# Performance work log

Hardware: AMD Instinct MI355X
Metric: run time of the kernel (lower is better)

## Reference

```python
import jax, jax.numpy as jnp
import numpy as np

# dims
B, T, HID = 2, 2048, 2048
HK, HV, DK, DV, KW = 16, 32, 128, 128, 4
KEY_DIM = HK * DK          # 2048
VAL_DIM = HV * DV          # 4096
CONV_DIM = 2 * KEY_DIM + VAL_DIM  # 8192
EPS = 1e-6


def setup_inputs() -> dict:
    key = jax.random.key(0)
    ks = jax.random.split(key, 10)
    s = 0.02
    return {
        "x": jax.random.normal(ks[0], (B, T, HID), jnp.float32),
        "input_pos": jnp.arange(T, dtype=jnp.int64),
        "W_qkv": jax.random.normal(ks[1], (CONV_DIM, HID), jnp.float32) * s,
        "W_z": jax.random.normal(ks[2], (VAL_DIM, HID), jnp.float32) * s,
        "W_b": jax.random.normal(ks[3], (HV, HID), jnp.float32) * s,
        "W_a": jax.random.normal(ks[4], (HV, HID), jnp.float32) * s,
        "conv_w": jax.random.normal(ks[5], (CONV_DIM, 1, KW), jnp.float32) * 0.2,
        "dt_bias": jnp.ones((HV,), jnp.float32),
        "A_log": jnp.log(jax.random.uniform(ks[6], (HV,), jnp.float32, 1e-3, 16.0)),
        "norm_weight": jnp.ones((DV,), jnp.float32),
        "W_out": jax.random.normal(ks[7], (HID, VAL_DIM), jnp.float32) * s,
    }


def _l2norm(t):
    n = jnp.sqrt(jnp.sum(t * t, axis=-1, keepdims=True))
    return t / jnp.maximum(n, 1e-12)


def _gdn_scan(q, k, v, g, beta):
    # per-batch: q,k [T,HV,DK], v [T,HV,DV], g,beta [T,HV]
    scale = DK ** -0.5
    def step(S, inp):  # S: [HV, DK, DV]
        qt, kt, vt, gt, bt = inp
        S = S * jnp.exp(gt)[:, None, None]
        kv = jnp.einsum('hk,hkv->hv', kt, S)
        S = S + jnp.einsum('hk,hv->hkv', kt, bt[:, None] * (vt - kv))
        o = jnp.einsum('hk,hkv->hv', qt * scale, S)
        return S, o
    S0 = jnp.zeros((HV, DK, DV), q.dtype)
    _, o = jax.lax.scan(step, S0, (q, k, v, g, beta))
    return o  # [T, HV, DV]


def reference(x, input_pos, W_qkv, W_z, W_b, W_a, conv_w, dt_bias, A_log, norm_weight, W_out):
    # conv_state / recurrent_state buffers start at zero (and input_pos[0]==0 resets them),
    # so the causal conv reduces to left-padded depthwise conv and the scan starts from S=0.
    mixed_qkv = jnp.einsum('bth,ch->btc', x, W_qkv)                    # [B,T,CONV_DIM]
    z = jnp.einsum('bth,vh->btv', x, W_z).reshape(B, T, HV, DV)
    beta = jax.nn.sigmoid(jnp.einsum('bth,nh->btn', x, W_b))           # [B,T,HV]
    a = jnp.einsum('bth,nh->btn', x, W_a)
    g = -jnp.exp(A_log) * jax.nn.softplus(a + dt_bias)                 # [B,T,HV]

    # causal depthwise conv1d over time
    xc = mixed_qkv.transpose(0, 2, 1)                                  # [B,C,T]
    yc = jax.lax.conv_general_dilated(
        xc, conv_w, window_strides=(1,), padding=[(KW - 1, 0)],
        dimension_numbers=('NCH', 'OIH', 'NCH'), feature_group_count=CONV_DIM)
    qkv = jax.nn.silu(yc).transpose(0, 2, 1)                           # [B,T,C]

    q = qkv[..., :KEY_DIM].reshape(B, T, HK, DK)
    k = qkv[..., KEY_DIM:2 * KEY_DIM].reshape(B, T, HK, DK)
    v = qkv[..., 2 * KEY_DIM:].reshape(B, T, HV, DV)
    q = _l2norm(q)
    k = _l2norm(k)
    rep = HV // HK
    q = jnp.repeat(q, rep, axis=2)                                     # [B,T,HV,DK]
    k = jnp.repeat(k, rep, axis=2)

    o = jax.vmap(_gdn_scan)(q, k, v, g, beta)                          # [B,T,HV,DV]

    # gated RMSNorm: RMSNorm(o) * weight * silu(z)
    of = o.astype(jnp.float32)
    normed = of * jax.lax.rsqrt(jnp.mean(of * of, axis=-1, keepdims=True) + EPS)
    out = (norm_weight * normed) * jax.nn.silu(z.astype(jnp.float32))
    out = out.reshape(B, T, VAL_DIM)
    return jnp.einsum('btv,hv->bth', out, W_out)
```

## Files before the change

### kernel.cpp

```cpp
#include <hip/hip_runtime.h>

#define BB 2
#define TT 2048
#define HID 2048
#define HK 16
#define HV 32
#define DK 128
#define DV 128
#define KW 4
#define KEY_DIM 2048
#define VAL_DIM 4096
#define CONV_DIM 8192
#define N1PAD 12544
#define M_ROWS 4096
#define CC 64

typedef __attribute__((ext_vector_type(8))) short short8;
typedef __attribute__((ext_vector_type(8))) unsigned short ushort8;
typedef __attribute__((ext_vector_type(4))) float f32x4;

__device__ __forceinline__ unsigned short f2bf(float f) {
  union { float f; unsigned int u; } v; v.f = f;
  unsigned int r = v.u + 0x7FFFu + ((v.u >> 16) & 1u);
  return (unsigned short)(r >> 16);
}
__device__ __forceinline__ float bf2f(unsigned short u) {
  union { unsigned int u; float f; } v; v.u = ((unsigned int)u) << 16; return v.f;
}

template <int CTRL>
__device__ __forceinline__ float dpp_add(float v) {
  union { float f; int i; } a, b;
  a.f = v;
  b.i = __builtin_amdgcn_update_dpp(0, a.i, CTRL, 0xf, 0xf, true);
  return a.f + b.f;
}
template <int CTRL>
__device__ __forceinline__ int dpp_mov(int v) {
  return __builtin_amdgcn_update_dpp(0, v, CTRL, 0xf, 0xf, true);
}
__device__ __forceinline__ float row16_sum(float v) {
  v = dpp_add<0xB1>(v); v = dpp_add<0x4E>(v);
  v = dpp_add<0x141>(v); v = dpp_add<0x140>(v);
  return v;
}
__device__ __forceinline__ float row8_sum(float v) {
  v = dpp_add<0xB1>(v); v = dpp_add<0x4E>(v); v = dpp_add<0x141>(v);
  return v;
}

__device__ __forceinline__ void gload_lds16(const unsigned short* g, unsigned short* l) {
  __builtin_amdgcn_global_load_lds((const __attribute__((address_space(1))) unsigned int*)g,
                                   (__attribute__((address_space(3))) unsigned int*)l,
                                   16, 0, 0);
}
__device__ __forceinline__ void gload_lds4(const float* g, unsigned short* l) {
  __builtin_amdgcn_global_load_lds((const __attribute__((address_space(1))) unsigned int*)g,
                                   (__attribute__((address_space(3))) unsigned int*)l,
                                   4, 0, 0);
}

__device__ __forceinline__ short8 ldswz8(const char* base, int row, int e16) {
  int L = (row << 8) + (e16 << 1);
  return *(const short8*)(base + (L ^ ((row & 7) << 4)));
}
__device__ __forceinline__ short8 ldswz7(const char* base, int row, int e16) {
  int L = (row << 7) + (e16 << 1);
  return *(const short8*)(base + (L ^ ((row & 7) << 4)));
}

__global__ void cvt_bf16(const float* __restrict__ in, unsigned short* __restrict__ out) {
  long i = ((long)blockIdx.x * 256 + threadIdx.x) * 4;
  float4 v = *(const float4*)&in[i];
  unsigned long long p = (unsigned long long)f2bf(v.x)
                       | ((unsigned long long)f2bf(v.y) << 16)
                       | ((unsigned long long)f2bf(v.z) << 32)
                       | ((unsigned long long)f2bf(v.w) << 48);
  *(unsigned long long*)&out[i] = p;
}

__global__ void build_wcat(const float* __restrict__ wqkv, const float* __restrict__ wz,
                           const float* __restrict__ wb, const float* __restrict__ wa,
                           unsigned short* __restrict__ wcat) {
  long idx = (long)blockIdx.x * 256 + threadIdx.x;
  long e = idx * 4;
  long r = e >> 11;
  int cc = (int)(e & 2047);
  unsigned long long p = 0ULL;
  if (r < 12352) {
    const float* src;
    if (r < 8192)       src = wqkv + r * 2048;
    else if (r < 12288) src = wz + (r - 8192) * 2048;
    else if (r < 12320) src = wb + (r - 12288) * 2048;
    else                src = wa + (r - 12320) * 2048;
    float4 v = *(const float4*)&src[cc];
    p = (unsigned long long)f2bf(v.x)
      | ((unsigned long long)f2bf(v.y) << 16)
      | ((unsigned long long)f2bf(v.z) << 32)
      | ((unsigned long long)f2bf(v.w) << 48);
  }
  *(unsigned long long*)&wcat[e] = p;
}

__device__ __forceinline__ void stage256(const unsigned short* __restrict__ G, long rb, int K,
                                         int kt, char* region, int r, int tid, int wid) {
  int i = r * 512 + tid;
  int row = i >> 3;
  int D = i << 4;
  int eb = (D ^ ((row & 7) << 4)) & 127;
  const unsigned short* src = G + (rb + row) * (long)K + kt * 64 + (eb >> 1);
  gload_lds16(src, (unsigned short*)region + r * 4096 + wid * 512);
}

__global__ __launch_bounds__(512, 2) void gemm256(const unsigned short* __restrict__ A,
                                                  const unsigned short* __restrict__ Bw,
                                                  unsigned short* __restrict__ Cout,
                                                  int N, int K) {
  extern __shared__ char gs[];
  const int tid = threadIdx.x, wid = tid >> 6, lane = tid & 63;
  const int lr = lane & 15, lq = lane >> 4;
  const long m0 = (long)blockIdx.y << 8;
  const long n0 = (long)blockIdx.x << 8;
  const int wr = wid >> 2, wc = wid & 3;
  const int nkt = K >> 6;

  f32x4 acc[8][4] = {};

#pragma unroll
  for (int r = 0; r < 4; ++r) {
    stage256(A, m0, K, 0, gs, r, tid, wid);
    stage256(Bw, n0, K, 0, gs + 32768, r, tid, wid);
  }
  asm volatile("s_waitcnt vmcnt(0)" ::: "memory");
  __syncthreads();

  for (int kt = 0; kt < nkt; ++kt) {
    char* cur = gs + ((kt & 1) << 16);
    char* nxt = gs + (((kt + 1) & 1) << 16);
    const char* cA = cur;
    const char* cB = cur + 32768;
    const bool pf = (kt + 1 < nkt);
    short8 bf[2][4];
#pragma unroll
    for (int p = 0; p < 4; ++p) {
      if (pf) {
        stage256(A, m0, K, kt + 1, nxt, p, tid, wid);
        stage256(Bw, n0, K, kt + 1, nxt + 32768, p, tid, wid);
      }
      if (p == 0) {
#pragma unroll
        for (int ks = 0; ks < 2; ++ks)
#pragma unroll
          for (int cf = 0; cf < 4; ++cf)
            bf[ks][cf] = ldswz7(cB, wc * 64 + cf * 16 + lr, ks * 32 + lq * 8);
      }
      short8 af[2][2];
#pragma unroll
      for (int ks = 0; ks < 2; ++ks)
#pragma unroll
        for (int rr = 0; rr < 2; ++rr)
          af[ks][rr] = ldswz7(cA, wr * 128 + (p * 2 + rr) * 16 + lr, ks * 32 + lq * 8);
      __builtin_amdgcn_s_setprio(1);
#pragma unroll
      for (int ks = 0; ks < 2; ++ks)
#pragma unroll
        for (int rr = 0; rr < 2; ++rr)
#pragma unroll
          for (int cf = 0; cf < 4; ++cf)
            acc[p * 2 + rr][cf] = __builtin_amdgcn_mfma_f32_16x16x32_bf16(
                af[ks][rr], bf[ks][cf], acc[p * 2 + rr][cf], 0, 0, 0);
      __builtin_amdgcn_s_setprio(0);
    }
    asm volatile("s_waitcnt vmcnt(0)" ::: "memory");
    __syncthreads();
  }

  const long rbase = m0 + wr * 128 + lq * 4;
  const long cbase = n0 + wc * 64 + lr;
#pragma unroll
  for (int rf = 0; rf < 8; ++rf)
#pragma unroll
    for (int cf = 0; cf < 4; ++cf)
#pragma unroll
      for (int j = 0; j < 4; ++j)
        Cout[(rbase + rf * 16 + j) * N + cbase + cf * 16] = f2bf(acc[rf][cf][j]);
}

template <bool BF16OUT>
__global__ __launch_bounds__(256) void gemm_bt(const unsigned short* __restrict__ A,
                                               const unsigned short* __restrict__ Bw,
                                               void* __restrict__ Cout,
                                               int N, int K) {
  __shared__ unsigned short lds[8192];
  const int tid = threadIdx.x;
  const int wid = tid >> 6;
  const int lane = tid & 63;
  const int m0 = blockIdx.y << 7;
  const int n0 = blockIdx.x << 7;
  const int wr = wid >> 1, wc = wid & 1;

  f32x4 acc[4][4] = {};

  const int srow = (wid << 4) + (lane >> 2);
  const int scol = (lane & 3) << 3;
  const unsigned short* gA0 = A + (long)(m0 + srow) * K + scol;
  const unsigned short* gA1 = A + (long)(m0 + 64 + srow) * K + scol;
  const unsigned short* gB0 = Bw + (long)(n0 + srow) * K + scol;
  const unsigned short* gB1 = Bw + (long)(n0 + 64 + srow) * K + scol;
  unsigned short* ldsA = &lds[wid << 9];
  unsigned short* ldsB = &lds[4096 + (wid << 9)];

  const int lrow = lane & 15;
  const int lk = (lane >> 4) << 3;

  for (int k0 = 0; k0 < K; k0 += 32) {
    __syncthreads();
    gload_lds16(gA0 + k0, ldsA);
    gload_lds16(gA1 + k0, ldsA + 2048);
    gload_lds16(gB0 + k0, ldsB);
    gload_lds16(gB1 + k0, ldsB + 2048);
    __syncthreads();
    short8 av[4], bv[4];
#pragma unroll
    for (int i = 0; i < 4; ++i) {
      av[i] = *(const short8*)&lds[((wr << 6) + (i << 4) + lrow) * 32 + lk];
      bv[i] = *(const short8*)&lds[4096 + ((wc << 6) + (i << 4) + lrow) * 32 + lk];
    }
#pragma unroll
    for (int i = 0; i < 4; ++i)
#pragma unroll
      for (int j = 0; j < 4; ++j)
        acc[i][j] = __builtin_amdgcn_mfma_f32_16x16x32_bf16(av[i], bv[j], acc[i][j], 0, 0, 0);
  }
  const int rbase = m0 + (wr << 6) + ((lane >> 4) << 2);
  const int cbase = n0 + (wc << 6) + (lane & 15);
#pragma unroll
  for (int i = 0; i < 4; ++i)
#pragma unroll
    for (int j = 0; j < 4; ++j)
#pragma unroll
      for (int r = 0; r < 4; ++r) {
        long idx = (long)(rbase + (i << 4) + r) * N + cbase + (j << 4);
        if (BF16OUT) ((unsigned short*)Cout)[idx] = f2bf(acc[i][j][r]);
        else         ((float*)Cout)[idx] = acc[i][j][r];
      }
}

__global__ __launch_bounds__(256) void conv_silu(const unsigned short* __restrict__ C1,
                                                 const float* __restrict__ convw,
                                                 unsigned short* __restrict__ qb,
                                                 unsigned short* __restrict__ kb,
                                                 unsigned short* __restrict__ vb) {
  const int bid = blockIdx.x;
  const int cb = bid & 3, tblk = (bid >> 2) & 63, b = bid >> 8;
  const int c0 = cb * 2048 + threadIdx.x * 8;
  float w0[8], w1[8], w2[8], w3[8];
#pragma unroll
  for (int j = 0; j < 8; ++j) {
    float4 wv = *(const float4*)&convw[(c0 + j) * 4];
    w0[j] = wv.x; w1[j] = wv.y; w2[j] = wv.z; w3[j] = wv.w;
  }
  const int t0 = tblk * 32;
  const long rowbase = ((long)b * TT) * N1PAD + c0;
  float x0[8], x1[8], x2[8];
#pragma unroll
  for (int j = 0; j < 8; ++j) { x0[j] = 0.f; x1[j] = 0.f; x2[j] = 0.f; }
  if (t0 >= 1) { ushort8 r = *(const ushort8*)&C1[rowbase + (long)(t0 - 1) * N1PAD];
#pragma unroll
    for (int j = 0; j < 8; ++j) x2[j] = bf2f(r[j]); }
  if (t0 >= 2) { ushort8 r = *(const ushort8*)&C1[rowbase + (long)(t0 - 2) * N1PAD];
#pragma unroll
    for (int j = 0; j < 8; ++j) x1[j] = bf2f(r[j]); }
  if (t0 >= 3) { ushort8 r = *(const ushort8*)&C1[rowbase + (long)(t0 - 3) * N1PAD];
#pragma unroll
    for (int j = 0; j < 8; ++j) x0[j] = bf2f(r[j]); }

  const float nsc = (cb == 0) ? 0.08838834764831845f : 1.0f;
  for (int t = t0; t < t0 + 32; ++t) {
    ushort8 rr = *(const ushort8*)&C1[rowbase + (long)t * N1PAD];
    float ys[8];
#pragma unroll
    for (int j = 0; j < 8; ++j) {
      float x3 = bf2f(rr[j]);
      float y = w0[j] * x0[j] + w1[j] * x1[j] + w2[j] * x2[j] + w3[j] * x3;
      ys[j] = y / (1.f + __expf(-y));
      x0[j] = x1[j]; x1[j] = x2[j]; x2[j] = x3;
    }
    if (cb < 2) {
      float ss = 0.f;
#pragma unroll
      for (int j = 0; j < 8; ++j) ss = fmaf(ys[j], ys[j], ss);
      ss = row16_sum(ss);
      float sc = nsc / fmaxf(sqrtf(ss), 1e-12f);
#pragma unroll
      for (int j = 0; j < 8; ++j) ys[j] *= sc;
    }
    ushort8 outp;
#pragma unroll
    for (int j = 0; j < 8; ++j) outp[j] = f2bf(ys[j]);
    long m = (long)b * TT + t;
    if (cb == 0)      *(ushort8*)&qb[m * 2048 + threadIdx.x * 8] = outp;
    else if (cb == 1) *(ushort8*)&kb[m * 2048 + threadIdx.x * 8] = outp;
    else              *(ushort8*)&vb[m * 4096 + (cb - 2) * 2048 + threadIdx.x * 8] = outp;
  }
}

__global__ void gbeta(const unsigned short* __restrict__ C1, const float* __restrict__ Alog,
                      const float* __restrict__ dtb, float* __restrict__ graw, float* __restrict__ betab) {
  int idx = blockIdx.x * 256 + threadIdx.x;
  int m = idx >> 5, h = idx & 31;
  float a = bf2f(C1[(long)m * N1PAD + 12320 + h]);
  float bl = bf2f(C1[(long)m * N1PAD + 12288 + h]);
  float xsp = a + dtb[h];
  float sp = (xsp > 20.f) ? xsp : log1pf(expf(xsp));
  graw[idx] = -expf(Alog[h]) * sp;
  betab[idx] = 1.f / (1.f + expf(-bl));
}

#define OFF_K   0
#define OFF_V   16384
#define OFF_G   20480
#define OFF_B2  20736
#define OFF_KT  20992
#define OFF_SH  37376
#define OFF_SL  45568
#define OFF_A2  53760
#define OFF_MM  71168
#define OFF_BT  79360
#define OFF_BT2 83456
#define OFF_X   87552
#define OFF_CS  96000
#define OFF_EXC 96256
#define OFF_ECT 96512
#define SMEM_SZ 96768

__global__ __launch_bounds__(512, 2) void chunk_scan(const unsigned short* __restrict__ qb,
                                                     const unsigned short* __restrict__ kb,
                                                     const unsigned short* __restrict__ vb,
                                                     const float* __restrict__ graw,
                                                     const float* __restrict__ betab,
                                                     unsigned short* __restrict__ ob) {
  extern __shared__ char smem[];
  const int w = blockIdx.x;
  const int rdec = w >> 5, gdec = w & 31;
  const int bat = gdec >> 4, hk = gdec & 15;
  const int h = hk * 2 + (rdec >> 2), vc = rdec & 3;
  const int tid = threadIdx.x, wid = tid >> 6, lane = tid & 63;
  const int lr = lane & 15, lq = lane >> 4;
  const int rg = wid & 3, half = wid >> 2;
  const int mr = wid & 1, nc2 = (wid >> 1) & 3;

  const long kqoff = ((long)bat * TT) * 2048 + hk * 128;
  const long voff  = ((long)bat * TT) * 4096 + h * 128 + vc * 32;
  const long goff  = ((long)bat * TT) * 32 + h;

  f32x4 Smast[2] = {};

  auto stage_full = [&](int t0c) {
#pragma unroll
    for (int it = 0; it < 2; ++it) {
      int i = it * 512 + tid;
      int row = i >> 4;
      int L = ((i & 15) << 4) ^ ((row & 7) << 4);
      long grow = (long)(t0c + row) * 2048 + (L >> 1);
      gload_lds16(kb + kqoff + grow, (unsigned short*)(smem + OFF_K) + it * 4096 + wid * 512);
    }
    if (tid < 256)
      gload_lds16(vb + voff + (long)(t0c + (tid >> 2)) * 4096 + (tid & 3) * 8,
                  (unsigned short*)(smem + OFF_V) + wid * 512);
    if (wid == 6) gload_lds4(graw  + goff + (long)(t0c + lane) * 32, (unsigned short*)(smem + OFF_G));
    if (wid == 7) gload_lds4(betab + goff + (long)(t0c + lane) * 32, (unsigned short*)(smem + OFF_B2));
  };
  auto stage_part = [&](int t0c) {
    int tid2 = tid - 256, wid2 = wid - 4;
#pragma unroll
    for (int it = 0; it < 4; ++it) {
      int i = it * 256 + tid2;
      int row = i >> 4;
      int L = ((i & 15) << 4) ^ ((row & 7) << 4);
      long grow = (long)(t0c + row) * 2048 + (L >> 1);
      gload_lds16(kb + kqoff + grow, (unsigned short*)(smem + OFF_K) + it * 2048 + wid2 * 512);
    }
    gload_lds16(vb + voff + (long)(t0c + (tid2 >> 2)) * 4096 + (tid2 & 3) * 8,
                (unsigned short*)(smem + OFF_V) + wid2 * 512);
    if (wid == 4) gload_lds4(graw  + goff + (long)(t0c + lane) * 32, (unsigned short*)(smem + OFF_G));
    if (wid == 5) gload_lds4(betab + goff + (long)(t0c + lane) * 32, (unsigned short*)(smem + OFF_B2));
  };
  auto loadQ = [&](short8 (&qr)[4], int t0c) {
#pragma unroll
    for (int kk = 0; kk < 4; ++kk)
      qr[kk] = *(const short8*)&qb[kqoff + (long)(t0c + 16 * rg + lr) * 2048 + kk * 32 + lq * 8];
  };

  auto body = [&](int ct, short8 (&qcur)[4], short8 (&qnext)[4]) {
    {
      int tp = tid & 31, dkb = tid >> 5;
      short8 r0 = ldswz8(smem + OFF_K, 2 * tp, dkb * 8);
      short8 r1 = ldswz8(smem + OFF_K, 2 * tp + 1, dkb * 8);
#pragma unroll
      for (int e = 0; e < 8; ++e) {
        int dk = dkb * 8 + e;
        unsigned int pk = (unsigned int)(unsigned short)r0[e]
                        | ((unsigned int)(unsigned short)r1[e] << 16);
        int Lk = (dk << 7) + (tp << 2);
        *(unsigned int*)(smem + OFF_KT + (Lk ^ ((dk & 7) << 4))) = pk;
      }
    }
    if (wid == 0) {
      float gv = ((const float*)(smem + OFF_G))[lane];
#pragma unroll
      for (int off = 1; off < 64; off <<= 1) {
        float n = __shfl_up(gv, off);
        if (lane >= off) gv += n;
      }
      ((float*)(smem + OFF_CS))[lane] = gv;
      ((float*)(smem + OFF_EXC))[lane] = __expf(gv);
      float tot = __shfl(gv, 63);
      ((float*)(smem + OFF_ECT))[lane] = __expf(tot - gv);
    }
    __syncthreads();

    f32x4 aKK[2] = {}, aQK[2] = {}, aKS = {}, aQS = {};
    float oq[4];
#pragma unroll
    for (int kk = 0; kk < 4; ++kk) {
      int ke = kk * 32 + lq * 8;
      short8 avk = ldswz8(smem + OFF_K, 16 * rg + lr, ke);
      short8 avq = qcur[kk];
#pragma unroll
      for (int tc2 = 0; tc2 < 2; ++tc2) {
        short8 bvk = ldswz8(smem + OFF_K, 16 * (2 * half + tc2) + lr, ke);
        aKK[tc2] = __builtin_amdgcn_mfma_f32_16x16x32_bf16(avk, bvk, aKK[tc2], 0, 0, 0);
        aQK[tc2] = __builtin_amdgcn_mfma_f32_16x16x32_bf16(avq, bvk, aQK[tc2], 0, 0, 0);
      }
      short8 bH = ldswz8(smem + OFF_SH, 16 * half + lr, ke);
      short8 bL = ldswz8(smem + OFF_SL, 16 * half + lr, ke);
      aKS = __builtin_amdgcn_mfma_f32_16x16x32_bf16(avk, bH, aKS, 0, 0, 0);
      aKS = __builtin_amdgcn_mfma_f32_16x16x32_bf16(avk, bL, aKS, 0, 0, 0);
      aQS = __builtin_amdgcn_mfma_f32_16x16x32_bf16(avq, bH, aQS, 0, 0, 0);
      aQS = __builtin_amdgcn_mfma_f32_16x16x32_bf16(avq, bL, aQS, 0, 0, 0);
    }
    {
      const float* csp  = (const float*)(smem + OFF_CS);
      const float* excp = (const float*)(smem + OFF_EXC);
      const float* betp = (const float*)(smem + OFF_B2);
      const unsigned short* vp = (const unsigned short*)(smem + OFF_V);
      float cst[4], bt4[4], ext[4];
#pragma unroll
      for (int j = 0; j < 4; ++j) {
        int t = 16 * rg + lq * 4 + j;
        cst[j] = csp[t]; bt4[j] = betp[t]; ext[j] = excp[t];
      }
#pragma unroll
      for (int tc2 = 0; tc2 < 2; ++tc2) {
        int i = 16 * (2 * half + tc2) + lr;
        float csi = csp[i];
#pragma unroll
        for (int j = 0; j < 4; ++j) {
          int t = 16 * rg + lq * 4 + j;
          float e = __expf(cst[j] - csi);
          float av = (i < t) ? bt4[j] * e * aKK[tc2][j] : 0.f;
          ((float*)(smem + OFF_A2))[t * 68 + (i & 7) * 8 + (i >> 3)] = av;
          float mv = (i <= t) ? e * aQK[tc2][j] : 0.f;
          unsigned int mvb = f2bf(mv);
          unsigned int mvp = (unsigned int)dpp_mov<0xB1>((int)mvb);
          if (!(lr & 1)) {
            int Lm = (t << 7) + (i << 1);
            *(unsigned int*)(smem + OFF_MM + (Lm ^ ((t & 7) << 4))) = mvb | (mvp << 16);
          }
        }
      }
      int vcl = 16 * half + lr;
#pragma unroll
      for (int j = 0; j < 4; ++j) {
        int t = 16 * rg + lq * 4 + j;
        float vvv = bf2f(vp[t * 32 + vcl]);
        float x = bt4[j] * (vvv - ext[j] * aKS[j]);
        ((float*)(smem + OFF_X))[t * 33 + vcl] = x;
        oq[j] = ext[j] * aQS[j];
      }
    }
    __syncthreads();

    if (ct + 1 < TT / CC) loadQ(qnext, (ct + 1) * CC);
    if (wid < 4) {
      const float* A2p  = (const float*)(smem + OFF_A2);
      const float* Xp   = (const float*)(smem + OFF_X);
      const float* ectp = (const float*)(smem + OFF_ECT);
      const int col = tid >> 3, rr = tid & 7;
      float bbv[8] = {0.f, 0.f, 0.f, 0.f, 0.f, 0.f, 0.f, 0.f};
#pragma unroll
      for (int t = 0; t < 64; ++t) {
        float4 a0 = *(const float4*)(A2p + t * 68 + rr * 8);
        float4 a1 = *(const float4*)(A2p + t * 68 + rr * 8 + 4);
        float sA = fmaf(a0.y, bbv[1], a0.x * bbv[0]);
        sA = fmaf(a0.z, bbv[2], sA); sA = fmaf(a0.w, bbv[3], sA);
        float sB = fmaf(a1.y, bbv[5], a1.x * bbv[4]);
        sB = fmaf(a1.z, bbv[6], sB); sB = fmaf(a1.w, bbv[7], sB);
        float s = row8_sum(sA + sB);
        float btv = Xp[t * 33 + col] - s;
        if (rr == (t & 7)) bbv[t >> 3] = btv;
      }
#pragma unroll
      for (int k = 0; k < 8; ++k) {
        int t = 8 * k + rr;
        int Lb = (col << 7) + (t << 1);
        int Pb = Lb ^ ((col & 7) << 4);
        *(unsigned short*)(smem + OFF_BT + Pb)  = f2bf(bbv[k]);
        *(unsigned short*)(smem + OFF_BT2 + Pb) = f2bf(bbv[k] * ectp[t]);
      }
    } else if (ct + 1 < TT / CC) {
      stage_part((ct + 1) * CC);
    }
    __syncthreads();

    {
      f32x4 accO = (f32x4){oq[0], oq[1], oq[2], oq[3]};
#pragma unroll
      for (int kk2 = 0; kk2 < 2; ++kk2) {
        int ke = kk2 * 32 + lq * 8;
        short8 aM = ldswz7(smem + OFF_MM, 16 * rg + lr, ke);
        short8 bB = ldswz7(smem + OFF_BT, 16 * half + lr, ke);
        accO = __builtin_amdgcn_mfma_f32_16x16x32_bf16(aM, bB, accO, 0, 0, 0);
      }
      int vcl = 16 * half + lr;
#pragma unroll
      for (int j = 0; j < 4; ++j) {
        int t = 16 * rg + lq * 4 + j;
        long tg = (long)(bat * TT + ct * CC + t);
        ob[(tg * 32 + h) * 128 + vc * 32 + vcl] = f2bf(accO[j]);
      }

      f32x4 accP[2] = {};
#pragma unroll
      for (int kk2 = 0; kk2 < 2; ++kk2) {
        int ke = kk2 * 32 + lq * 8;
        short8 aB2 = ldswz7(smem + OFF_BT2, 16 * mr + lr, ke);
#pragma unroll
        for (int c4 = 0; c4 < 2; ++c4) {
          short8 bK = ldswz7(smem + OFF_KT, 16 * (2 * nc2 + c4) + lr, ke);
          accP[c4] = __builtin_amdgcn_mfma_f32_16x16x32_bf16(aB2, bK, accP[c4], 0, 0, 0);
        }
      }
      float ecC = ((const float*)(smem + OFF_EXC))[63];
#pragma unroll
      for (int c4 = 0; c4 < 2; ++c4)
#pragma unroll
        for (int j = 0; j < 4; ++j) {
          float sv = fmaf(ecC, Smast[c4][j], accP[c4][j]);
          Smast[c4][j] = sv;
          int vcr = 16 * mr + lq * 4 + j;
          int dk  = 16 * (2 * nc2 + c4) + lr;
          unsigned int hi = f2bf(sv);
          unsigned int lo = f2bf(sv - bf2f((unsigned short)hi));
          unsigned int hip = (unsigned int)dpp_mov<0xB1>((int)hi);
          unsigned int lop = (unsigned int)dpp_mov<0xB1>((int)lo);
          if (!(lr & 1)) {
            int Ls = (vcr << 8) + (dk << 1);
            int Ps = Ls ^ ((vcr & 7) << 4);
            *(unsigned int*)(smem + OFF_SH + Ps) = hi | (hip << 16);
            *(unsigned int*)(smem + OFF_SL + Ps) = lo | (lop << 16);
          }
        }
    }
    asm volatile("s_waitcnt vmcnt(0)" ::: "memory");
    __syncthreads();
  };

  short8 qA[4], qB[4];
  loadQ(qA, 0);
  stage_full(0);
  *(f32x4*)(smem + OFF_SH + tid * 32)      = (f32x4){0.f, 0.f, 0.f, 0.f};
  *(f32x4*)(smem + OFF_SH + tid * 32 + 16) = (f32x4){0.f, 0.f, 0.f, 0.f};
  asm volatile("s_waitcnt vmcnt(0)" ::: "memory");
  __syncthreads();

  for (int cp = 0; cp < TT / CC / 2; ++cp) {
    body(2 * cp, qA, qB);
    body(2 * cp + 1, qB, qA);
  }
}

__global__ __launch_bounds__(256) void norm_silu(const unsigned short* __restrict__ ob,
                                                 const unsigned short* __restrict__ C1,
                                                 const float* __restrict__ nw,
                                                 unsigned short* __restrict__ nrm) {
  int unit = blockIdx.x * 4 + (threadIdx.x >> 6);
  int lane = threadIdx.x & 63;
  int m = unit >> 5, h = unit & 31;
  unsigned int uo = *(const unsigned int*)&ob[(long)unit * 128 + lane * 2];
  float o0 = bf2f((unsigned short)(uo & 0xffff));
  float o1 = bf2f((unsigned short)(uo >> 16));
  float ss = o0 * o0 + o1 * o1;
#pragma unroll
  for (int mm = 1; mm < 64; mm <<= 1) ss += __shfl_xor(ss, mm);
  float rs = rsqrtf(ss * (1.0f / 128.0f) + 1e-6f);
  unsigned int uz = *(const unsigned int*)&C1[(long)m * N1PAD + 8192 + h * 128 + lane * 2];
  float z0 = bf2f((unsigned short)(uz & 0xffff));
  float z1 = bf2f((unsigned short)(uz >> 16));
  float s0 = z0 / (1.f + expf(-z0));
  float s1 = z1 / (1.f + expf(-z1));
  float r0 = o0 * rs * nw[lane * 2] * s0;
  float r1 = o1 * rs * nw[lane * 2 + 1] * s1;
  unsigned int pk = (unsigned int)f2bf(r0) | ((unsigned int)f2bf(r1) << 16);
  *(unsigned int*)&nrm[(long)unit * 128 + lane * 2] = pk;
}

extern "C" void kernel_launch(void* const* d_in, const int* in_sizes, int n_in,
                              void* d_out, int out_size, void* d_ws, size_t ws_size,
                              hipStream_t stream) {
  const float* x    = (const float*)d_in[0];
  const float* Wqkv = (const float*)d_in[2];
  const float* Wz   = (const float*)d_in[3];
  const float* Wb   = (const float*)d_in[4];
  const float* Wa   = (const float*)d_in[5];
  const float* convw= (const float*)d_in[6];
  const float* dtb  = (const float*)d_in[7];
  const float* Alog = (const float*)d_in[8];
  const float* nw   = (const float*)d_in[9];
  const float* Wout = (const float*)d_in[10];
  float* out = (float*)d_out;

  char* ws = (char*)d_ws;
  const size_t OFF_C1    = 0;
  const size_t OFF_XB    = 102760448;
  const size_t OFF_WCAT  = 119537664;
  const size_t OFF_QB    = OFF_XB;
  const size_t OFF_KB    = 119537664;
  const size_t OFF_VB    = 136314880;
  const size_t OFF_EG    = 170917888;
  const size_t OFF_BE    = 171442176;
  const size_t OFF_OB    = 171966464;
  const size_t OFF_NRM   = OFF_QB;
  const size_t OFF_WOUTB = OFF_VB;

  unsigned short* C1    = (unsigned short*)(ws + OFF_C1);
  unsigned short* xb    = (unsigned short*)(ws + OFF_XB);
  unsigned short* wcat  = (unsigned short*)(ws + OFF_WCAT);
  unsigned short* qbuf  = (unsigned short*)(ws + OFF_QB);
  unsigned short* kbuf  = (unsigned short*)(ws + OFF_KB);
  unsigned short* vbuf  = (unsigned short*)(ws + OFF_VB);
  float*          egb   = (float*)(ws + OFF_EG);
  float*          betab = (float*)(ws + OFF_BE);
  unsigned short* obuf  = (unsigned short*)(ws + OFF_OB);
  unsigned short* nrm   = (unsigned short*)(ws + OFF_NRM);
  unsigned short* woutb = (unsigned short*)(ws + OFF_WOUTB);
  (void)ws_size; (void)in_sizes; (void)n_in; (void)out_size;

  static int smem_set = 0;
  if (!smem_set) {
    hipFuncSetAttribute(reinterpret_cast<const void*>(chunk_scan),
                        hipFuncAttributeMaxDynamicSharedMemorySize, SMEM_SZ);
    hipFuncSetAttribute(reinterpret_cast<const void*>(gemm256),
                        hipFuncAttributeMaxDynamicSharedMemorySize, 131072);
    smem_set = 1;
  }

  cvt_bf16<<<8192, 256, 0, stream>>>(x, xb);
  build_wcat<<<25088, 256, 0, stream>>>(Wqkv, Wz, Wb, Wa, wcat);
  gemm256<<<dim3(N1PAD / 256, M_ROWS / 256), 512, 131072, stream>>>(xb, wcat, C1, N1PAD, 2048);
  conv_silu<<<512, 256, 0, stream>>>(C1, convw, qbuf, kbuf, vbuf);
  gbeta<<<512, 256, 0, stream>>>(C1, Alog, dtb, egb, betab);
  chunk_scan<<<256, 512, SMEM_SZ, stream>>>(qbuf, kbuf, vbuf, egb, betab, obuf);
  cvt_bf16<<<8192, 256, 0, stream>>>(Wout, woutb);
  norm_silu<<<32768, 256, 0, stream>>>(obuf, C1, nw, nrm);
  gemm_bt<false><<<dim3(2048 / 128, M_ROWS / 128), 256, 0, stream>>>(nrm, woutb, out, 2048, 4096);
}
```

Before: 784.0 us.

## Replace output GEMM with double-buffered 128x256 pipelined kernel; hoist X loads in solve

The output projection GEMM now uses a 512-thread, 128x256 tile kernel with double-buffered swizzled LDS staging. The next K-tile is prefetched while MFMAs run on the current one, replacing the simple single-buffered 128x128 kernel with two barriers per 32-wide K step. The chunk scan's triangular solve also preloads its X values into registers before the loop instead of reading LDS every iteration. This trades more LDS per block and more registers for better latency hiding.

Result: faster. 718.8 us, median of 4 (-8.3%).

```diff
diff --git a/kernel.cpp b/kernel.cpp
--- a/kernel.cpp
+++ b/kernel.cpp
@@ -186,64 +186,73 @@
         Cout[(rbase + rf * 16 + j) * N + cbase + cf * 16] = f2bf(acc[rf][cf][j]);
 }
 
-template <bool BF16OUT>
-__global__ __launch_bounds__(256) void gemm_bt(const unsigned short* __restrict__ A,
-                                               const unsigned short* __restrict__ Bw,
-                                               void* __restrict__ Cout,
-                                               int N, int K) {
-  __shared__ unsigned short lds[8192];
-  const int tid = threadIdx.x;
-  const int wid = tid >> 6;
-  const int lane = tid & 63;
-  const int m0 = blockIdx.y << 7;
-  const int n0 = blockIdx.x << 7;
-  const int wr = wid >> 1, wc = wid & 1;
+__global__ __launch_bounds__(512, 2) void gemm128x256(const unsigned short* __restrict__ A,
+                                                      const unsigned short* __restrict__ Bw,
+                                                      float* __restrict__ Cout,
+                                                      int N, int K) {
+  extern __shared__ char gs[];
+  const int tid = threadIdx.x, wid = tid >> 6, lane = tid & 63;
+  const int lr = lane & 15, lq = lane >> 4;
+  const long m0 = (long)blockIdx.y << 7;
+  const long n0 = (long)blockIdx.x << 8;
+  const int wr = wid >> 2, wc = wid & 3;
+  const int nkt = K >> 6;
 
   f32x4 acc[4][4] = {};
 
-  const int srow = (wid << 4) + (lane >> 2);
-  const int scol = (lane & 3) << 3;
-  const unsigned short* gA0 = A + (long)(m0 + srow) * K + scol;
-  const unsigned short* gA1 = A + (long)(m0 + 64 + srow) * K + scol;
-  const unsigned short* gB0 = Bw + (long)(n0 + srow) * K + scol;
-  const unsigned short* gB1 = Bw + (long)(n0 + 64 + srow) * K + scol;
-  unsigned short* ldsA = &lds[wid << 9];
-  unsigned short* ldsB = &lds[4096 + (wid << 9)];
-
-  const int lrow = lane & 15;
-  const int lk = (lane >> 4) << 3;
-
-  for (int k0 = 0; k0 < K; k0 += 32) {
+#pragma unroll
+  for (int r = 0; r < 2; ++r) stage256(A, m0, K, 0, gs, r, tid, wid);
+#pragma unroll
+  for (int r = 0; r < 4; ++r) stage256(Bw, n0, K, 0, gs + 16384, r, tid, wid);
+  asm volatile("s_waitcnt vmcnt(0)" ::: "memory");
+  __syncthreads();
+
+  for (int kt = 0; kt < nkt; ++kt) {
+    char* cur = gs + (kt & 1) * 49152;
+    char* nxt = gs + ((kt + 1) & 1) * 49152;
+    const char* cA = cur;
+    const char* cB = cur + 16384;
+    const bool pf = (kt + 1 < nkt);
+    short8 bf[2][4];
+#pragma unroll
+    for (int p = 0; p < 4; ++p) {
+      if (pf) {
+        if (p < 2) stage256(A, m0, K, kt + 1, nxt, p, tid, wid);
+        stage256(Bw, n0, K, kt + 1, nxt + 16384, p, tid, wid);
+      }
+      if (p == 0) {
+#pragma unroll
+        for (int ks = 0; ks < 2; ++ks)
+#pragma unroll
+          for (int cf = 0; cf < 4; ++cf)
+            bf[ks][cf] = ldswz7(cB, wc * 64 + cf * 16 + lr, ks * 32 + lq * 8);
+      }
+      short8 af[2];
+#pragma unroll
+      for (int ks = 0; ks < 2; ++ks)
+        af[ks] = ldswz7(cA, wr * 64 + p * 16 + lr, ks * 32 + lq * 8);
+      __builtin_amdgcn_s_setprio(1);
+#pragma unroll
+      for (int ks = 0; ks < 2; ++ks)
+#pragma unroll
+        for (int cf = 0; cf < 4; ++cf)
+          acc[p][cf] = __builtin_amdgcn_mfma_f32_16x16x32_bf16(
+              af[ks], bf[ks][cf], acc[p][cf], 0, 0, 0);
+      __builtin_amdgcn_s_setprio(0);
+    }
+    asm volatile("s_waitcnt vmcnt(0)" ::: "memory");
     __syncthreads();
-    gload_lds16(gA0 + k0, ldsA);
-    gload_lds16(gA1 + k0, ldsA + 2048);
-    gload_lds16(gB0 + k0, ldsB);
-    gload_lds16(gB1 + k0, ldsB + 2048);
-    __syncthreads();
-    short8 av[4], bv[4];
-#pragma unroll
-    for (int i = 0; i < 4; ++i) {
-      av[i] = *(const short8*)&lds[((wr << 6) + (i << 4) + lrow) * 32 + lk];
-      bv[i] = *(const short8*)&lds[4096 + ((wc << 6) + (i << 4) + lrow) * 32 + lk];
-    }
-#pragma unroll
-    for (int i = 0; i < 4; ++i)
+  }
+
+  const long rbase = m0 + wr * 64 + lq * 4;
+  const long cbase = n0 + wc * 64 + lr;
+#pragma unroll
+  for (int rf = 0; rf < 4; ++rf)
+#pragma unroll
+    for (int cf = 0; cf < 4; ++cf)
 #pragma unroll
       for (int j = 0; j < 4; ++j)
-        acc[i][j] = __builtin_amdgcn_mfma_f32_16x16x32_bf16(av[i], bv[j], acc[i][j], 0, 0, 0);
-  }
-  const int rbase = m0 + (wr << 6) + ((lane >> 4) << 2);
-  const int cbase = n0 + (wc << 6) + (lane & 15);
-#pragma unroll
-  for (int i = 0; i < 4; ++i)
-#pragma unroll
-    for (int j = 0; j < 4; ++j)
-#pragma unroll
-      for (int r = 0; r < 4; ++r) {
-        long idx = (long)(rbase + (i << 4) + r) * N + cbase + (j << 4);
-        if (BF16OUT) ((unsigned short*)Cout)[idx] = f2bf(acc[i][j][r]);
-        else         ((float*)Cout)[idx] = acc[i][j][r];
-      }
+        Cout[(rbase + rf * 16 + j) * N + cbase + cf * 16] = acc[rf][cf][j];
 }
 
 __global__ __launch_bounds__(256) void conv_silu(const unsigned short* __restrict__ C1,
@@ -488,6 +497,9 @@
       const float* Xp   = (const float*)(smem + OFF_X);
       const float* ectp = (const float*)(smem + OFF_ECT);
       const int col = tid >> 3, rr = tid & 7;
+      float bbvX[8];
+#pragma unroll
+      for (int k = 0; k < 8; ++k) bbvX[k] = Xp[(8 * k + rr) * 33 + col];
       float bbv[8] = {0.f, 0.f, 0.f, 0.f, 0.f, 0.f, 0.f, 0.f};
 #pragma unroll
       for (int t = 0; t < 64; ++t) {
@@ -498,7 +510,7 @@
         float sB = fmaf(a1.y, bbv[5], a1.x * bbv[4]);
         sB = fmaf(a1.z, bbv[6], sB); sB = fmaf(a1.w, bbv[7], sB);
         float s = row8_sum(sA + sB);
-        float btv = Xp[t * 33 + col] - s;
+        float btv = bbvX[t >> 3] - s;
         if (rr == (t & 7)) bbv[t >> 3] = btv;
       }
 #pragma unroll
@@ -653,6 +665,8 @@
                         hipFuncAttributeMaxDynamicSharedMemorySize, SMEM_SZ);
     hipFuncSetAttribute(reinterpret_cast<const void*>(gemm256),
                         hipFuncAttributeMaxDynamicSharedMemorySize, 131072);
+    hipFuncSetAttribute(reinterpret_cast<const void*>(gemm128x256),
+                        hipFuncAttributeMaxDynamicSharedMemorySize, 98304);
     smem_set = 1;
   }
 
@@ -664,5 +678,5 @@
   chunk_scan<<<256, 512, SMEM_SZ, stream>>>(qbuf, kbuf, vbuf, egb, betab, obuf);
   cvt_bf16<<<8192, 256, 0, stream>>>(Wout, woutb);
   norm_silu<<<32768, 256, 0, stream>>>(obuf, C1, nw, nrm);
-  gemm_bt<false><<<dim3(2048 / 128, M_ROWS / 128), 256, 0, stream>>>(nrm, woutb, out, 2048, 4096);
-}
+  gemm128x256<<<dim3(2048 / 256, M_ROWS / 128), 512, 98304, stream>>>(nrm, woutb, out, 2048, 4096);
+}
```
